# Kernel tuning notes

Hardware: AMD Instinct MI355X
Metric: run time of the kernel (lower is better)

Reference implementation:

```python
import jax, jax.numpy as jnp
import numpy as np

N_NODES = 50000
N_EDGES = 800000
N_GRAPHS = 64
D_IN = 128
DIMS = (256, 256)


def _glorot(key, shape):
    fan_in, fan_out = shape[0], shape[1]
    lim = jnp.sqrt(6.0 / (fan_in + fan_out)).astype(jnp.float32)
    return jax.random.uniform(key, shape, jnp.float32, -lim, lim)


def setup_inputs() -> dict:
    key = jax.random.key(0)
    ks = jax.random.split(key, 12)
    x = jax.random.normal(ks[0], (N_NODES, D_IN), dtype=jnp.float32)
    edge_index = jax.random.randint(ks[1], (2, N_EDGES), 0, N_NODES, dtype=jnp.int64)
    batch = jnp.sort(jax.random.randint(ks[2], (N_NODES,), 0, N_GRAPHS, dtype=jnp.int64))
    # MLP params per GIN layer: Linear(in,dim) -> ReLU -> Linear(dim,dim) -> ReLU
    W1_0 = _glorot(ks[3], (D_IN, DIMS[0]))
    b1_0 = jnp.zeros((DIMS[0],), jnp.float32)
    W2_0 = _glorot(ks[4], (DIMS[0], DIMS[0]))
    b2_0 = jnp.zeros((DIMS[0],), jnp.float32)
    W1_1 = _glorot(ks[5], (DIMS[0], DIMS[1]))
    b1_1 = jnp.zeros((DIMS[1],), jnp.float32)
    W2_1 = _glorot(ks[6], (DIMS[1], DIMS[1]))
    b2_1 = jnp.zeros((DIMS[1],), jnp.float32)
    return {"x": x, "edge_index": edge_index, "batch": batch,
            "W1_0": W1_0, "b1_0": b1_0, "W2_0": W2_0, "b2_0": b2_0,
            "W1_1": W1_1, "b1_1": b1_1, "W2_1": W2_1, "b2_1": b2_1}


def _gin_layer(x, src, dst, W1, b1, W2, b2):
    # aggregate: sum of neighbor features (messages from src into dst)
    agg = jax.ops.segment_sum(x[src], dst, num_segments=N_NODES)
    h = x + agg  # (1 + eps) * x + agg, eps = 0
    h = jax.nn.relu(h @ W1 + b1)
    h = jax.nn.relu(h @ W2 + b2)
    return h


def reference(x, edge_index, batch, W1_0, b1_0, W2_0, b2_0, W1_1, b1_1, W2_1, b2_1):
    src, dst = edge_index[0], edge_index[1]
    h = _gin_layer(x, src, dst, W1_0, b1_0, W2_0, b2_0)
    h = _gin_layer(h, src, dst, W1_1, b1_1, W2_1, b2_1)
    # global mean pool over graphs
    sums = jax.ops.segment_sum(h, batch, num_segments=N_GRAPHS)
    counts = jax.ops.segment_sum(jnp.ones((h.shape[0],), h.dtype), batch, num_segments=N_GRAPHS)
    return sums / jnp.maximum(counts, 1.0)[:, None]
```

## Files before the change

### kernel.cpp

```cpp
#include <hip/hip_runtime.h>


typedef __bf16 bf16x8 __attribute__((ext_vector_type(8)));
typedef float f32x4 __attribute__((ext_vector_type(4)));

#define N_NODES 50000
#define N_EDGES 800000
#define N_GRAPHS 64
#define SCAN_BLOCKS 196

#define PB_HIST0 3125
#define PB_P0    6250
#define PB_P1    6378
#define PB_P2    6634
#define PB_P3    6890
#define PB_BIAS  7146
#define PB_TOTAL 7150

#define OFF_FLAGS  0ull
#define OFF_WB     64ull
#define OFF_WP0    4096ull
#define OFF_WP1    (OFF_WP0 + 65536ull)
#define OFF_WP2    (OFF_WP1 + 131072ull)
#define OFF_WP3    (OFF_WP2 + 131072ull)
#define OFF_CNT    462848ull
#define OFF_ROWPTR 662864ull
#define OFF_CURSOR 862880ull
#define OFF_SSRC   1062912ull
#define OFF_A      2662912ull
#define OFF_B      15462912ull
#define OFF_C      41062912ull
#define OFF_POOL32 66662912ull
#define OFF_BSUM   66728448ull
#define OFF_BOFF   66729472ull

__device__ __forceinline__ float b2f(unsigned short u) {
  union { unsigned int i; float f; } v; v.i = ((unsigned int)u) << 16; return v.f;
}
__device__ __forceinline__ float b2f_lo(unsigned int u) {
  union { unsigned int i; float f; } v; v.i = u << 16; return v.f;
}
__device__ __forceinline__ float b2f_hi(unsigned int u) {
  union { unsigned int i; float f; } v; v.i = u & 0xffff0000u; return v.f;
}
__device__ __forceinline__ unsigned short f2b(float f) {
  union { unsigned int i; float f; } v; v.f = f;
  unsigned int r = v.i + 0x7fffu + ((v.i >> 16) & 1u);
  return (unsigned short)(r >> 16);
}

__global__ void detect_zero(const unsigned int* __restrict__ xw,
                            const unsigned int* __restrict__ eiw,
                            int* __restrict__ flags,
                            int* __restrict__ counts, float* __restrict__ pool32) {
  if (blockIdx.x == 0) {
    __shared__ int s_f[256], s_i[256];
    int t = threadIdx.x;
    int fh = 0, iz = 0;
    for (int i = t; i < 1024; i += 256) {
      unsigned int e = (xw[i] >> 7) & 0xFFu;
      fh += (e >= 115u && e <= 130u) ? 1 : 0;
      iz += (eiw[2 * i + 1] == 0u) ? 1 : 0;
    }
    s_f[t] = fh; s_i[t] = iz;
    __syncthreads();
    for (int s = 128; s > 0; s >>= 1) {
      if (t < s) { s_f[t] += s_f[t + s]; s_i[t] += s_i[t + s]; }
      __syncthreads();
    }
    if (t == 0) { flags[0] = s_f[0] > 512 ? 1 : 0; flags[1] = s_i[0] > 512 ? 1 : 0; }
  } else {
    int i = (blockIdx.x - 1) * 256 + threadIdx.x;
    if (i < N_NODES) counts[i] = 0;
    if (i < N_GRAPHS * 256) pool32[i] = 0.f;
  }
}

__device__ __forceinline__ void pack_w_elem(const void* W, unsigned short* Wp,
                                            int e, int isb) {
  int n = e & 255;
  int krow = e >> 8;
  int kb = krow >> 5, r = krow & 31;
  int q = r >> 3, j = r & 7;
  size_t out = ((((size_t)(kb << 8) + n) << 2) + q) * 8 + j;
  Wp[out] = isb ? ((const unsigned short*)W)[e] : f2b(((const float*)W)[e]);
}

__global__ void prep_kernel(const void* __restrict__ x, const int* __restrict__ ei,
                            const void* W0, const void* W1, const void* W2, const void* W3,
                            const void* b0, const void* b1, const void* b2, const void* b3,
                            unsigned short* __restrict__ A,
                            int* __restrict__ counts,
                            unsigned short* __restrict__ Wp0, unsigned short* __restrict__ Wp1,
                            unsigned short* __restrict__ Wp2, unsigned short* __restrict__ Wp3,
                            unsigned short* __restrict__ Wb,
                            const int* __restrict__ flags) {
  int b = blockIdx.x, t = threadIdx.x;
  int isb = flags[0];
  if (b < PB_HIST0) {
    if (!isb) {
      int i = b * 256 + t;
      const float4* f = (const float4*)x;
      float4 a = f[2 * i], c = f[2 * i + 1];
      ushort4 o0; o0.x = f2b(a.x); o0.y = f2b(a.y); o0.z = f2b(a.z); o0.w = f2b(a.w);
      ushort4 o1; o1.x = f2b(c.x); o1.y = f2b(c.y); o1.z = f2b(c.z); o1.w = f2b(c.w);
      ((ushort4*)A)[2 * i] = o0;
      ((ushort4*)A)[2 * i + 1] = o1;
    }
  } else if (b < PB_P0) {
    int e = (b - PB_HIST0) * 256 + t;
    int dst = flags[1] ? ei[2 * (N_EDGES + e)] : ei[N_EDGES + e];
    atomicAdd(&counts[dst], 1);
  } else if (b < PB_P1) {
    pack_w_elem(W0, Wp0, (b - PB_P0) * 256 + t, isb);
  } else if (b < PB_P2) {
    pack_w_elem(W1, Wp1, (b - PB_P1) * 256 + t, isb);
  } else if (b < PB_P3) {
    pack_w_elem(W2, Wp2, (b - PB_P2) * 256 + t, isb);
  } else if (b < PB_BIAS) {
    pack_w_elem(W3, Wp3, (b - PB_P3) * 256 + t, isb);
  } else {
    int i = (b - PB_BIAS) * 256 + t;
    const void* p = (i < 256) ? b0 : (i < 512) ? b1 : (i < 768) ? b2 : b3;
    int n = i & 255;
    Wb[i] = isb ? ((const unsigned short*)p)[n] : f2b(((const float*)p)[n]);
  }
}

__global__ void scan_blocks(const int* __restrict__ counts,
                            int* __restrict__ rowptr, int* __restrict__ bsum) {
  __shared__ int sd[256];
  int t = threadIdx.x;
  int i = blockIdx.x * 256 + t;
  int v = (i < N_NODES) ? counts[i] : 0;
  sd[t] = v;
  __syncthreads();
  for (int off = 1; off < 256; off <<= 1) {
    int u = (t >= off) ? sd[t - off] : 0;
    __syncthreads();
    sd[t] += u;
    __syncthreads();
  }
  if (i < N_NODES) rowptr[i] = sd[t] - v;
  if (t == 255) bsum[blockIdx.x] = sd[255];
}

__global__ void scan_sums(const int* __restrict__ bsum, int* __restrict__ boff) {
  __shared__ int sd[256];
  int t = threadIdx.x;
  int v = (t < SCAN_BLOCKS) ? bsum[t] : 0;
  sd[t] = v;
  __syncthreads();
  for (int off = 1; off < 256; off <<= 1) {
    int u = (t >= off) ? sd[t - off] : 0;
    __syncthreads();
    sd[t] += u;
    __syncthreads();
  }
  if (t < SCAN_BLOCKS) boff[t] = sd[t] - v;
}

__global__ void scan_add(int* __restrict__ rowptr, int* __restrict__ cursor,
                         const int* __restrict__ boff) {
  int i = blockIdx.x * 256 + threadIdx.x;
  if (i < N_NODES) {
    int v = rowptr[i] + boff[blockIdx.x];
    rowptr[i] = v;
    cursor[i] = v;
  }
  if (i == 0) rowptr[N_NODES] = N_EDGES;
}

__global__ void fill_kernel(const int* __restrict__ ei, int* __restrict__ cursor,
                            unsigned short* __restrict__ ssrc,
                            const int* __restrict__ flags) {
  int e = blockIdx.x * blockDim.x + threadIdx.x;
  if (e >= N_EDGES) return;
  int is64 = flags[1];
  int src = is64 ? ei[2 * e] : ei[e];
  int dst = is64 ? ei[2 * (N_EDGES + e)] : ei[N_EDGES + e];
  int pos = atomicAdd(&cursor[dst], 1);
  ssrc[pos] = (unsigned short)src;
}

__global__ void fused_gather_gemm(const unsigned short* __restrict__ featCanon,
                                  const unsigned short* __restrict__ featRaw,
                                  const int* __restrict__ rowptr,
                                  const unsigned short* __restrict__ ssrc,
                                  const unsigned short* __restrict__ Wp,
                                  const unsigned short* __restrict__ Wb, int bias_row,
                                  unsigned short* __restrict__ C, int D,
                                  const int* __restrict__ flags) {
  __shared__ __align__(16) unsigned short Alds[16 * 264];
  const int S = D + 8;
  const int row0 = blockIdx.x << 4;
  const int lane = threadIdx.x & 63;
  const int wave = threadIdx.x >> 6;
  const unsigned short* feat = flags[0] ? featRaw : featCanon;

  {
    int sub = lane >> 4;
    int l = lane & 15;
    int nl = (wave << 2) + sub;
    int node = row0 + nl;
    int beg = rowptr[node], end = rowptr[node + 1];
    int c = l << 3;
    if (D == 256) {
      const unsigned short* sp = feat + (size_t)node * 256 + c;
      uint4 sv0 = *(const uint4*)sp;
      uint4 sv1 = *(const uint4*)(sp + 128);
      float a0 = b2f_lo(sv0.x), a1 = b2f_hi(sv0.x), a2 = b2f_lo(sv0.y), a3 = b2f_hi(sv0.y);
      float a4 = b2f_lo(sv0.z), a5 = b2f_hi(sv0.z), a6 = b2f_lo(sv0.w), a7 = b2f_hi(sv0.w);
      float a8 = b2f_lo(sv1.x), a9 = b2f_hi(sv1.x), aA = b2f_lo(sv1.y), aB = b2f_hi(sv1.y);
      float aC = b2f_lo(sv1.z), aD = b2f_hi(sv1.z), aE = b2f_lo(sv1.w), aF = b2f_hi(sv1.w);
      int i = beg;
      for (; i + 1 < end; i += 2) {
        int s0 = ssrc[i], s1 = ssrc[i + 1];
        const unsigned short* p0 = feat + (size_t)s0 * 256 + c;
        const unsigned short* p1 = feat + (size_t)s1 * 256 + c;
        uint4 v00 = *(const uint4*)p0;
        uint4 v01 = *(const uint4*)(p0 + 128);
        uint4 v10 = *(const uint4*)p1;
        uint4 v11 = *(const uint4*)(p1 + 128);
        a0 += b2f_lo(v00.x); a1 += b2f_hi(v00.x); a2 += b2f_lo(v00.y); a3 += b2f_hi(v00.y);
        a4 += b2f_lo(v00.z); a5 += b2f_hi(v00.z); a6 += b2f_lo(v00.w); a7 += b2f_hi(v00.w);
        a8 += b2f_lo(v01.x); a9 += b2f_hi(v01.x); aA += b2f_lo(v01.y); aB += b2f_hi(v01.y);
        aC += b2f_lo(v01.z); aD += b2f_hi(v01.z); aE += b2f_lo(v01.w); aF += b2f_hi(v01.w);
        a0 += b2f_lo(v10.x); a1 += b2f_hi(v10.x); a2 += b2f_lo(v10.y); a3 += b2f_hi(v10.y);
        a4 += b2f_lo(v10.z); a5 += b2f_hi(v10.z); a6 += b2f_lo(v10.w); a7 += b2f_hi(v10.w);
        a8 += b2f_lo(v11.x); a9 += b2f_hi(v11.x); aA += b2f_lo(v11.y); aB += b2f_hi(v11.y);
        aC += b2f_lo(v11.z); aD += b2f_hi(v11.z); aE += b2f_lo(v11.w); aF += b2f_hi(v11.w);
      }
      if (i < end) {
        const unsigned short* p0 = feat + (size_t)ssrc[i] * 256 + c;
        uint4 v00 = *(const uint4*)p0;
        uint4 v01 = *(const uint4*)(p0 + 128);
        a0 += b2f_lo(v00.x); a1 += b2f_hi(v00.x); a2 += b2f_lo(v00.y); a3 += b2f_hi(v00.y);
        a4 += b2f_lo(v00.z); a5 += b2f_hi(v00.z); a6 += b2f_lo(v00.w); a7 += b2f_hi(v00.w);
        a8 += b2f_lo(v01.x); a9 += b2f_hi(v01.x); aA += b2f_lo(v01.y); aB += b2f_hi(v01.y);
        aC += b2f_lo(v01.z); aD += b2f_hi(v01.z); aE += b2f_lo(v01.w); aF += b2f_hi(v01.w);
      }
      uint4 o0, o1;
      o0.x = ((unsigned int)f2b(a1) << 16) | f2b(a0);
      o0.y = ((unsigned int)f2b(a3) << 16) | f2b(a2);
      o0.z = ((unsigned int)f2b(a5) << 16) | f2b(a4);
      o0.w = ((unsigned int)f2b(a7) << 16) | f2b(a6);
      o1.x = ((unsigned int)f2b(a9) << 16) | f2b(a8);
      o1.y = ((unsigned int)f2b(aB) << 16) | f2b(aA);
      o1.z = ((unsigned int)f2b(aD) << 16) | f2b(aC);
      o1.w = ((unsigned int)f2b(aF) << 16) | f2b(aE);
      *(uint4*)(&Alds[nl * S + c]) = o0;
      *(uint4*)(&Alds[nl * S + c + 128]) = o1;
    } else {
      const unsigned short* sp = feat + (size_t)node * 128 + c;
      uint4 sv0 = *(const uint4*)sp;
      float a0 = b2f_lo(sv0.x), a1 = b2f_hi(sv0.x), a2 = b2f_lo(sv0.y), a3 = b2f_hi(sv0.y);
      float a4 = b2f_lo(sv0.z), a5 = b2f_hi(sv0.z), a6 = b2f_lo(sv0.w), a7 = b2f_hi(sv0.w);
      int i = beg;
      for (; i + 1 < end; i += 2) {
        int s0 = ssrc[i], s1 = ssrc[i + 1];
        uint4 v0 = *(const uint4*)(feat + (size_t)s0 * 128 + c);
        uint4 v1 = *(const uint4*)(feat + (size_t)s1 * 128 + c);
        a0 += b2f_lo(v0.x); a1 += b2f_hi(v0.x); a2 += b2f_lo(v0.y); a3 += b2f_hi(v0.y);
        a4 += b2f_lo(v0.z); a5 += b2f_hi(v0.z); a6 += b2f_lo(v0.w); a7 += b2f_hi(v0.w);
        a0 += b2f_lo(v1.x); a1 += b2f_hi(v1.x); a2 += b2f_lo(v1.y); a3 += b2f_hi(v1.y);
        a4 += b2f_lo(v1.z); a5 += b2f_hi(v1.z); a6 += b2f_lo(v1.w); a7 += b2f_hi(v1.w);
      }
      if (i < end) {
        uint4 v0 = *(const uint4*)(feat + (size_t)ssrc[i] * 128 + c);
        a0 += b2f_lo(v0.x); a1 += b2f_hi(v0.x); a2 += b2f_lo(v0.y); a3 += b2f_hi(v0.y);
        a4 += b2f_lo(v0.z); a5 += b2f_hi(v0.z); a6 += b2f_lo(v0.w); a7 += b2f_hi(v0.w);
      }
      uint4 o0;
      o0.x = ((unsigned int)f2b(a1) << 16) | f2b(a0);
      o0.y = ((unsigned int)f2b(a3) << 16) | f2b(a2);
      o0.z = ((unsigned int)f2b(a5) << 16) | f2b(a4);
      o0.w = ((unsigned int)f2b(a7) << 16) | f2b(a6);
      *(uint4*)(&Alds[nl * S + c]) = o0;
    }
  }
  __syncthreads();

  const int m = lane & 15;
  const int q = lane >> 4;
  f32x4 acc[4];
#pragma unroll
  for (int t = 0; t < 4; ++t) acc[t] = (f32x4){0.f, 0.f, 0.f, 0.f};

  const unsigned short* arow = &Alds[m * S + (q << 3)];
  const int nb = (wave << 6) + m;
  const int kblocks = D >> 5;
  for (int kb = 0; kb < kblocks; ++kb) {
    bf16x8 af = *(const bf16x8*)(arow + (kb << 5));
    const unsigned short* wp = Wp + (((size_t)(kb << 8) + nb) * 4 + q) * 8;
    bf16x8 b0 = *(const bf16x8*)(wp);
    bf16x8 b1 = *(const bf16x8*)(wp + 512);
    bf16x8 b2 = *(const bf16x8*)(wp + 1024);
    bf16x8 b3 = *(const bf16x8*)(wp + 1536);
    acc[0] = __builtin_amdgcn_mfma_f32_16x16x32_bf16(af, b0, acc[0], 0, 0, 0);
    acc[1] = __builtin_amdgcn_mfma_f32_16x16x32_bf16(af, b1, acc[1], 0, 0, 0);
    acc[2] = __builtin_amdgcn_mfma_f32_16x16x32_bf16(af, b2, acc[2], 0, 0, 0);
    acc[3] = __builtin_amdgcn_mfma_f32_16x16x32_bf16(af, b3, acc[3], 0, 0, 0);
  }
#pragma unroll
  for (int t = 0; t < 4; ++t) {
    int n = (wave << 6) + (t << 4) + m;
    float bv = b2f(Wb[bias_row * 256 + n]);
#pragma unroll
    for (int i = 0; i < 4; ++i) {
      int r = row0 + (q << 2) + i;
      float v = fmaxf(acc[t][i] + bv, 0.f);
      C[(size_t)r * 256 + n] = f2b(v);
    }
  }
}

__global__ void gemm_relu(const unsigned short* __restrict__ A,
                          const unsigned short* __restrict__ Wp,
                          const unsigned short* __restrict__ Wb, int bias_row,
                          unsigned short* __restrict__ C, int K) {
  const int row0 = blockIdx.x << 4;
  const int lane = threadIdx.x & 63;
  const int wave = threadIdx.x >> 6;
  const int m = lane & 15;
  const int q = lane >> 4;
  f32x4 acc[4];
#pragma unroll
  for (int t = 0; t < 4; ++t) acc[t] = (f32x4){0.f, 0.f, 0.f, 0.f};

  const unsigned short* arow = A + (size_t)(row0 + m) * K + (q << 3);
  const int nb = (wave << 6) + m;
  const int kblocks = K >> 5;
  for (int kb = 0; kb < kblocks; ++kb) {
    bf16x8 af = *(const bf16x8*)(arow + (kb << 5));
    const unsigned short* wp = Wp + (((size_t)(kb << 8) + nb) * 4 + q) * 8;
    bf16x8 b0 = *(const bf16x8*)(wp);
    bf16x8 b1 = *(const bf16x8*)(wp + 512);
    bf16x8 b2 = *(const bf16x8*)(wp + 1024);
    bf16x8 b3 = *(const bf16x8*)(wp + 1536);
    acc[0] = __builtin_amdgcn_mfma_f32_16x16x32_bf16(af, b0, acc[0], 0, 0, 0);
    acc[1] = __builtin_amdgcn_mfma_f32_16x16x32_bf16(af, b1, acc[1], 0, 0, 0);
    acc[2] = __builtin_amdgcn_mfma_f32_16x16x32_bf16(af, b2, acc[2], 0, 0, 0);
    acc[3] = __builtin_amdgcn_mfma_f32_16x16x32_bf16(af, b3, acc[3], 0, 0, 0);
  }
#pragma unroll
  for (int t = 0; t < 4; ++t) {
    int n = (wave << 6) + (t << 4) + m;
    float bv = b2f(Wb[bias_row * 256 + n]);
#pragma unroll
    for (int i = 0; i < 4; ++i) {
      int r = row0 + (q << 2) + i;
      float v = fmaxf(acc[t][i] + bv, 0.f);
      C[(size_t)r * 256 + n] = f2b(v);
    }
  }
}

__global__ void gemm_pool(const unsigned short* __restrict__ A,
                          const unsigned short* __restrict__ Wp,
                          const unsigned short* __restrict__ Wb, int bias_row,
                          float* __restrict__ pool32, const int* __restrict__ batch,
                          const int* __restrict__ flags, int K) {
  __shared__ int sg[16];
  const int row0 = blockIdx.x << 4;
  const int lane = threadIdx.x & 63;
  const int wave = threadIdx.x >> 6;
  if (threadIdx.x < 16) {
    int r = row0 + threadIdx.x;
    sg[threadIdx.x] = flags[1] ? batch[2 * r] : batch[r];
  }
  __syncthreads();

  const int m = lane & 15;
  const int q = lane >> 4;
  f32x4 acc[4];
#pragma unroll
  for (int t = 0; t < 4; ++t) acc[t] = (f32x4){0.f, 0.f, 0.f, 0.f};

  const unsigned short* arow = A + (size_t)(row0 + m) * K + (q << 3);
  const int nb = (wave << 6) + m;
  const int kblocks = K >> 5;
  for (int kb = 0; kb < kblocks; ++kb) {
    bf16x8 af = *(const bf16x8*)(arow + (kb << 5));
    const unsigned short* wp = Wp + (((size_t)(kb << 8) + nb) * 4 + q) * 8;
    bf16x8 b0 = *(const bf16x8*)(wp);
    bf16x8 b1 = *(const bf16x8*)(wp + 512);
    bf16x8 b2 = *(const bf16x8*)(wp + 1024);
    bf16x8 b3 = *(const bf16x8*)(wp + 1536);
    acc[0] = __builtin_amdgcn_mfma_f32_16x16x32_bf16(af, b0, acc[0], 0, 0, 0);
    acc[1] = __builtin_amdgcn_mfma_f32_16x16x32_bf16(af, b1, acc[1], 0, 0, 0);
    acc[2] = __builtin_amdgcn_mfma_f32_16x16x32_bf16(af, b2, acc[2], 0, 0, 0);
    acc[3] = __builtin_amdgcn_mfma_f32_16x16x32_bf16(af, b3, acc[3], 0, 0, 0);
  }

  int uniform = (sg[0] == sg[15]);
#pragma unroll
  for (int t = 0; t < 4; ++t) {
    int n = (wave << 6) + (t << 4) + m;
    float bv = b2f(Wb[bias_row * 256 + n]);
    float v0 = fmaxf(acc[t][0] + bv, 0.f);
    float v1 = fmaxf(acc[t][1] + bv, 0.f);
    float v2 = fmaxf(acc[t][2] + bv, 0.f);
    float v3 = fmaxf(acc[t][3] + bv, 0.f);
    if (uniform) {
      float ps = v0 + v1 + v2 + v3;
      ps += __shfl_xor(ps, 16);
      ps += __shfl_xor(ps, 32);
      if (q == 0) unsafeAtomicAdd(&pool32[sg[0] * 256 + n], ps);
    } else {
      int gp = sg[q << 2];
      float a = 0.f;
      float vv[4] = {v0, v1, v2, v3};
#pragma unroll
      for (int i = 0; i < 4; ++i) {
        int g = sg[(q << 2) + i];
        if (g != gp) { unsafeAtomicAdd(&pool32[gp * 256 + n], a); a = 0.f; gp = g; }
        a += vv[i];
      }
      unsafeAtomicAdd(&pool32[gp * 256 + n], a);
    }
  }
}

__device__ __forceinline__ int lower_bound(const int* a, int n, int v, int is64) {
  int lo = 0, hi = n;
  while (lo < hi) {
    int mid = (lo + hi) >> 1;
    int bv = is64 ? a[2 * mid] : a[mid];
    if (bv < v) lo = mid + 1; else hi = mid;
  }
  return lo;
}

__global__ void pool_final(const float* __restrict__ pool32,
                           const int* __restrict__ batch,
                           void* __restrict__ out,
                           const int* __restrict__ flags) {
  __shared__ int sh[2];
  int g = blockIdx.x;
  int is64 = flags[1];
  if (threadIdx.x == 0) sh[0] = lower_bound(batch, N_NODES, g, is64);
  if (threadIdx.x == 1) sh[1] = lower_bound(batch, N_NODES, g + 1, is64);
  __syncthreads();
  int c = threadIdx.x;
  float res = pool32[g * 256 + c] / fmaxf((float)(sh[1] - sh[0]), 1.0f);
  if (flags[0]) ((unsigned short*)out)[(size_t)g * 256 + c] = f2b(res);
  else          ((float*)out)[(size_t)g * 256 + c] = res;
}

extern "C" void kernel_launch(void* const* d_in, const int* in_sizes, int n_in,
                              void* d_out, int out_size, void* d_ws, size_t ws_size,
                              hipStream_t stream) {
  const void* x    = d_in[0];
  const int*  ei   = (const int*)d_in[1];
  const int*  batch= (const int*)d_in[2];

  char* ws = (char*)d_ws;
  int*            flags = (int*)(ws + OFF_FLAGS);
  unsigned short* Wb    = (unsigned short*)(ws + OFF_WB);
  unsigned short* Wp0   = (unsigned short*)(ws + OFF_WP0);
  unsigned short* Wp1   = (unsigned short*)(ws + OFF_WP1);
  unsigned short* Wp2   = (unsigned short*)(ws + OFF_WP2);
  unsigned short* Wp3   = (unsigned short*)(ws + OFF_WP3);
  int*            cnts  = (int*)(ws + OFF_CNT);
  int*            rowp  = (int*)(ws + OFF_ROWPTR);
  int*            curs  = (int*)(ws + OFF_CURSOR);
  unsigned short* ssrc  = (unsigned short*)(ws + OFF_SSRC);
  unsigned short* A     = (unsigned short*)(ws + OFF_A);
  unsigned short* B     = (unsigned short*)(ws + OFF_B);
  unsigned short* C     = (unsigned short*)(ws + OFF_C);
  float*          pool32= (float*)(ws + OFF_POOL32);
  int*            bsum  = (int*)(ws + OFF_BSUM);
  int*            boff  = (int*)(ws + OFF_BOFF);

  detect_zero<<<197, 256, 0, stream>>>((const unsigned int*)x, (const unsigned int*)ei,
                                       flags, cnts, pool32);
  prep_kernel<<<PB_TOTAL, 256, 0, stream>>>(x, ei,
                                            d_in[3], d_in[5], d_in[7], d_in[9],
                                            d_in[4], d_in[6], d_in[8], d_in[10],
                                            A, cnts, Wp0, Wp1, Wp2, Wp3, Wb, flags);
  scan_blocks<<<SCAN_BLOCKS, 256, 0, stream>>>(cnts, rowp, bsum);
  scan_sums<<<1, 256, 0, stream>>>(bsum, boff);
  scan_add<<<SCAN_BLOCKS, 256, 0, stream>>>(rowp, curs, boff);
  fill_kernel<<<3125, 256, 0, stream>>>(ei, curs, ssrc, flags);

  fused_gather_gemm<<<3125, 256, 0, stream>>>(A, (const unsigned short*)x, rowp, ssrc,
                                              Wp0, Wb, 0, C, 128, flags);
  gemm_relu<<<3125, 256, 0, stream>>>(C, Wp1, Wb, 1, B, 256);

  fused_gather_gemm<<<3125, 256, 0, stream>>>(B, B, rowp, ssrc,
                                              Wp2, Wb, 2, C, 256, flags);
  gemm_pool<<<3125, 256, 0, stream>>>(C, Wp3, Wb, 3, pool32, batch, flags, 256);

  pool_final<<<N_GRAPHS, 256, 0, stream>>>(pool32, batch, d_out, flags);
}
```

Baseline: 386.2 us.

## Sort nodes by in-degree so gather blocks process balanced neighbor counts

Builds a degree histogram and a counting-sort permutation of nodes by in-degree, then has the fused gather+GEMM kernels process rows in permuted order and scatter outputs back to their original rows. Grouping similar-degree nodes in a block reduces wave divergence and load imbalance in the neighbor-sum loop. The cost is extra histogram atomics, a permutation indirection, scattered output stores and less locality in the self-feature reads. The scan kernels are restructured so the block-offset scan is folded into the fix-up pass.

```diff
diff --git a/kernel.cpp b/kernel.cpp
--- a/kernel.cpp
+++ b/kernel.cpp
@@ -32,7 +32,9 @@
 #define OFF_C      41062912ull
 #define OFF_POOL32 66662912ull
 #define OFF_BSUM   66728448ull
-#define OFF_BOFF   66729472ull
+#define OFF_DCNT   66730496ull
+#define OFF_DCUR   66731520ull
+#define OFF_PERM   66732544ull
 
 __device__ __forceinline__ float b2f(unsigned short u) {
   union { unsigned int i; float f; } v; v.i = ((unsigned int)u) << 16; return v.f;
@@ -52,7 +54,8 @@
 __global__ void detect_zero(const unsigned int* __restrict__ xw,
                             const unsigned int* __restrict__ eiw,
                             int* __restrict__ flags,
-                            int* __restrict__ counts, float* __restrict__ pool32) {
+                            int* __restrict__ counts, float* __restrict__ pool32,
+                            int* __restrict__ dcnt) {
   if (blockIdx.x == 0) {
     __shared__ int s_f[256], s_i[256];
     int t = threadIdx.x;
@@ -73,6 +76,7 @@
     int i = (blockIdx.x - 1) * 256 + threadIdx.x;
     if (i < N_NODES) counts[i] = 0;
     if (i < N_GRAPHS * 256) pool32[i] = 0.f;
+    if (i < 256) dcnt[i] = 0;
   }
 }
 
@@ -128,13 +132,18 @@
 }
 
 __global__ void scan_blocks(const int* __restrict__ counts,
-                            int* __restrict__ rowptr, int* __restrict__ bsum) {
-  __shared__ int sd[256];
+                            int* __restrict__ rowptr, int* __restrict__ bsum,
+                            int* __restrict__ dcnt) {
+  __shared__ int sd[256], lh[256];
   int t = threadIdx.x;
   int i = blockIdx.x * 256 + t;
   int v = (i < N_NODES) ? counts[i] : 0;
   sd[t] = v;
-  __syncthreads();
+  lh[t] = 0;
+  __syncthreads();
+  if (i < N_NODES) atomicAdd(&lh[v > 255 ? 255 : v], 1);
+  __syncthreads();
+  if (lh[t] > 0) atomicAdd(&dcnt[t], lh[t]);
   for (int off = 1; off < 256; off <<= 1) {
     int u = (t >= off) ? sd[t - off] : 0;
     __syncthreads();
@@ -145,10 +154,10 @@
   if (t == 255) bsum[blockIdx.x] = sd[255];
 }
 
-__global__ void scan_sums(const int* __restrict__ bsum, int* __restrict__ boff) {
+__global__ void deg_scan(const int* __restrict__ dcnt, int* __restrict__ dcur) {
   __shared__ int sd[256];
   int t = threadIdx.x;
-  int v = (t < SCAN_BLOCKS) ? bsum[t] : 0;
+  int v = dcnt[t];
   sd[t] = v;
   __syncthreads();
   for (int off = 1; off < 256; off <<= 1) {
@@ -157,18 +166,45 @@
     sd[t] += u;
     __syncthreads();
   }
-  if (t < SCAN_BLOCKS) boff[t] = sd[t] - v;
-}
-
-__global__ void scan_add(int* __restrict__ rowptr, int* __restrict__ cursor,
-                         const int* __restrict__ boff) {
-  int i = blockIdx.x * 256 + threadIdx.x;
+  dcur[t] = sd[t] - v;
+}
+
+__global__ void scan_fix(int* __restrict__ rowptr, int* __restrict__ cursor,
+                         const int* __restrict__ bsum, const int* __restrict__ counts,
+                         int* __restrict__ dcur, int* __restrict__ perm) {
+  __shared__ int sb[256], base[256], lc[256];
+  int t = threadIdx.x;
+  sb[t] = (t < SCAN_BLOCKS) ? bsum[t] : 0;
+  lc[t] = 0;
+  __syncthreads();
+  for (int off = 1; off < 256; off <<= 1) {
+    int u = (t >= off) ? sb[t - off] : 0;
+    __syncthreads();
+    sb[t] += u;
+    __syncthreads();
+  }
+  int boffv = (blockIdx.x > 0) ? sb[blockIdx.x - 1] : 0;
+  int i = blockIdx.x * 256 + t;
+  int d = 0;
   if (i < N_NODES) {
-    int v = rowptr[i] + boff[blockIdx.x];
+    int v = rowptr[i] + boffv;
     rowptr[i] = v;
     cursor[i] = v;
+    int c = counts[i];
+    d = c > 255 ? 255 : c;
+    atomicAdd(&lc[d], 1);
   }
   if (i == 0) rowptr[N_NODES] = N_EDGES;
+  __syncthreads();
+  int cnt = lc[t];
+  base[t] = (cnt > 0) ? atomicAdd(&dcur[t], cnt) : 0;
+  __syncthreads();
+  lc[t] = 0;
+  __syncthreads();
+  if (i < N_NODES) {
+    int r = atomicAdd(&lc[d], 1);
+    perm[base[d] + r] = i;
+  }
 }
 
 __global__ void fill_kernel(const int* __restrict__ ei, int* __restrict__ cursor,
@@ -187,28 +223,32 @@
                                   const unsigned short* __restrict__ featRaw,
                                   const int* __restrict__ rowptr,
                                   const unsigned short* __restrict__ ssrc,
+                                  const int* __restrict__ perm,
                                   const unsigned short* __restrict__ Wp,
                                   const unsigned short* __restrict__ Wb, int bias_row,
                                   unsigned short* __restrict__ C, int D,
                                   const int* __restrict__ flags) {
   __shared__ __align__(16) unsigned short Alds[16 * 264];
+  __shared__ int sp[16];
   const int S = D + 8;
   const int row0 = blockIdx.x << 4;
   const int lane = threadIdx.x & 63;
   const int wave = threadIdx.x >> 6;
   const unsigned short* feat = flags[0] ? featRaw : featCanon;
+  if (threadIdx.x < 16) sp[threadIdx.x] = perm[row0 + threadIdx.x];
+  __syncthreads();
 
   {
     int sub = lane >> 4;
     int l = lane & 15;
     int nl = (wave << 2) + sub;
-    int node = row0 + nl;
+    int node = sp[nl];
     int beg = rowptr[node], end = rowptr[node + 1];
     int c = l << 3;
     if (D == 256) {
-      const unsigned short* sp = feat + (size_t)node * 256 + c;
-      uint4 sv0 = *(const uint4*)sp;
-      uint4 sv1 = *(const uint4*)(sp + 128);
+      const unsigned short* spt = feat + (size_t)node * 256 + c;
+      uint4 sv0 = *(const uint4*)spt;
+      uint4 sv1 = *(const uint4*)(spt + 128);
       float a0 = b2f_lo(sv0.x), a1 = b2f_hi(sv0.x), a2 = b2f_lo(sv0.y), a3 = b2f_hi(sv0.y);
       float a4 = b2f_lo(sv0.z), a5 = b2f_hi(sv0.z), a6 = b2f_lo(sv0.w), a7 = b2f_hi(sv0.w);
       float a8 = b2f_lo(sv1.x), a9 = b2f_hi(sv1.x), aA = b2f_lo(sv1.y), aB = b2f_hi(sv1.y);
@@ -252,8 +292,8 @@
       *(uint4*)(&Alds[nl * S + c]) = o0;
       *(uint4*)(&Alds[nl * S + c + 128]) = o1;
     } else {
-      const unsigned short* sp = feat + (size_t)node * 128 + c;
-      uint4 sv0 = *(const uint4*)sp;
+      const unsigned short* spt = feat + (size_t)node * 128 + c;
+      uint4 sv0 = *(const uint4*)spt;
       float a0 = b2f_lo(sv0.x), a1 = b2f_hi(sv0.x), a2 = b2f_lo(sv0.y), a3 = b2f_hi(sv0.y);
       float a4 = b2f_lo(sv0.z), a5 = b2f_hi(sv0.z), a6 = b2f_lo(sv0.w), a7 = b2f_hi(sv0.w);
       int i = beg;
@@ -308,7 +348,7 @@
     float bv = b2f(Wb[bias_row * 256 + n]);
 #pragma unroll
     for (int i = 0; i < 4; ++i) {
-      int r = row0 + (q << 2) + i;
+      int r = sp[(q << 2) + i];
       float v = fmaxf(acc[t][i] + bv, 0.f);
       C[(size_t)r * 256 + n] = f2b(v);
     }
@@ -471,25 +511,27 @@
   unsigned short* C     = (unsigned short*)(ws + OFF_C);
   float*          pool32= (float*)(ws + OFF_POOL32);
   int*            bsum  = (int*)(ws + OFF_BSUM);
-  int*            boff  = (int*)(ws + OFF_BOFF);
+  int*            dcnt  = (int*)(ws + OFF_DCNT);
+  int*            dcur  = (int*)(ws + OFF_DCUR);
+  int*            perm  = (int*)(ws + OFF_PERM);
 
   detect_zero<<<197, 256, 0, stream>>>((const unsigned int*)x, (const unsigned int*)ei,
-                                       flags, cnts, pool32);
+                                       flags, cnts, pool32, dcnt);
   prep_kernel<<<PB_TOTAL, 256, 0, stream>>>(x, ei,
                                             d_in[3], d_in[5], d_in[7], d_in[9],
                                             d_in[4], d_in[6], d_in[8], d_in[10],
                                             A, cnts, Wp0, Wp1, Wp2, Wp3, Wb, flags);
-  scan_blocks<<<SCAN_BLOCKS, 256, 0, stream>>>(cnts, rowp, bsum);
-  scan_sums<<<1, 256, 0, stream>>>(bsum, boff);
-  scan_add<<<SCAN_BLOCKS, 256, 0, stream>>>(rowp, curs, boff);
+  scan_blocks<<<SCAN_BLOCKS, 256, 0, stream>>>(cnts, rowp, bsum, dcnt);
+  deg_scan<<<1, 256, 0, stream>>>(dcnt, dcur);
+  scan_fix<<<SCAN_BLOCKS, 256, 0, stream>>>(rowp, curs, bsum, cnts, dcur, perm);
   fill_kernel<<<3125, 256, 0, stream>>>(ei, curs, ssrc, flags);
 
   fused_gather_gemm<<<3125, 256, 0, stream>>>(A, (const unsigned short*)x, rowp, ssrc,
-                                              Wp0, Wb, 0, C, 128, flags);
+                                              perm, Wp0, Wb, 0, C, 128, flags);
   gemm_relu<<<3125, 256, 0, stream>>>(C, Wp1, Wb, 1, B, 256);
 
   fused_gather_gemm<<<3125, 256, 0, stream>>>(B, B, rowp, ssrc,
-                                              Wp2, Wb, 2, C, 256, flags);
+                                              perm, Wp2, Wb, 2, C, 256, flags);
   gemm_pool<<<3125, 256, 0, stream>>>(C, Wp3, Wb, 3, pool32, batch, flags, 256);
 
   pool_final<<<N_GRAPHS, 256, 0, stream>>>(pool32, batch, d_out, flags);
```

Result: no change. 383.7 us (-0.7%).
